# Optimization experiments

Measured on AMD Instinct MI355X. Metric: run time of the kernel, lower is better.

Reference implementation:

```python
import jax, jax.numpy as jnp
import numpy as np

B, S, DIM = 4, 2048, 1024
H, DH = 16, 64
INNER = H * DH  # 1024
SCALE = DH ** -0.5
NEG = -10000.0


def setup_inputs() -> dict:
    key = jax.random.key(0)
    k1, k2, k3, k4 = jax.random.split(key, 4)
    x = jax.random.normal(k1, (B, S, DIM), dtype=jnp.float32)
    w_qkv = jax.random.normal(k2, (DIM, 3 * INNER), dtype=jnp.float32) * (DIM ** -0.5)
    w_out = jax.random.normal(k3, (INNER, DIM), dtype=jnp.float32) * (INNER ** -0.5)
    b_out = jax.random.normal(k4, (DIM,), dtype=jnp.float32) * 0.01
    return {"x": x, "w_qkv": w_qkv, "w_out": w_out, "b_out": b_out}


def reference(x, w_qkv, w_out, b_out):
    b, s, _ = x.shape
    qkv = x @ w_qkv                                  # [b, s, 3*inner]
    q, k, v = jnp.split(qkv, 3, axis=-1)
    def heads(t):
        return t.reshape(b, s, H, DH).transpose(0, 2, 1, 3)  # [b, h, s, dh]
    q, k, v = heads(q), heads(k), heads(v)
    sim = jnp.einsum('bhid,bhjd->bhij', q, k)        # [b, h, s, s]
    i = jnp.arange(s)
    mask = jnp.where(i[None, :] <= i[:, None], 0.0, NEG).astype(sim.dtype)
    # NOTE: original scales (sim + mask), so mask bias is -10000*scale
    attn = jax.nn.softmax((sim + mask) * SCALE, axis=-1)
    out = jnp.einsum('bhij,bhjd->bhid', attn, v)     # [b, h, s, dh]
    out = out.transpose(0, 2, 1, 3).reshape(b, s, INNER)
    return out @ w_out + b_out
```

## Files before the change

kernel.cpp:

```cpp
#include <hip/hip_runtime.h>
#include <stdint.h>

typedef unsigned short u16;
typedef uint32_t u32;
typedef __attribute__((ext_vector_type(4))) float f32x4;
typedef __attribute__((ext_vector_type(16))) float f32x16;
typedef __attribute__((ext_vector_type(8))) short bf16x8;
typedef __attribute__((ext_vector_type(4))) u32 u32x4;

#define MFMA16(a,b,c) __builtin_amdgcn_mfma_f32_16x16x32_bf16((a),(b),(c),0,0,0)
#define MFMA32(a,b,c) __builtin_amdgcn_mfma_f32_32x32x16_bf16((a),(b),(c),0,0,0)
#define QSCALE 0.18033688011112042f
#define MASKB  -1803.3688011112042f
#define MBASE  -16.0f

__device__ __forceinline__ u16 f2bf(float f){
  union { float f; uint32_t u; } v; v.f = f;
  uint32_t r = v.u + 0x7fffu + ((v.u >> 16) & 1u);
  return (u16)(r >> 16);
}

__device__ __forceinline__ u32 cvtpk(float lo, float hi){
  u32 r;
  asm volatile("v_cvt_pk_bf16_f32 %0, %1, %2" : "=v"(r) : "v"(lo), "v"(hi));
  return r;
}

__device__ __forceinline__ void plswap(u32 &a, u32 &b){
  auto r = __builtin_amdgcn_permlane32_swap(a, b, false, false);
  union { decltype(r) v; u32 w[2]; } u; u.v = r;
  a = u.w[0]; b = u.w[1];
}

union U4 { u32x4 u; bf16x8 b; };
__device__ __forceinline__ bf16x8 mkfrag(u32 a, u32 b, u32 c, u32 d){
  U4 x; x.u = (u32x4){a,b,c,d}; return x.b;
}

__device__ __forceinline__ void gload16(const void* g, void* l){
  __builtin_amdgcn_global_load_lds(
      (const __attribute__((address_space(1))) void*)g,
      (__attribute__((address_space(3))) void*)l, 16, 0, 0);
}

__global__ __launch_bounds__(256) void prep_k(const float* __restrict__ x, u16* __restrict__ xb,
                                              const float* __restrict__ w_qkv, u16* __restrict__ wqkvT,
                                              const float* __restrict__ w_out, u16* __restrict__ woutT){
  __shared__ float tile[64][65];
  const int id = blockIdx.x, t = threadIdx.x;
  if (id < 8192){
    int i = id*256 + t;
    float4 v = reinterpret_cast<const float4*>(x)[i];
    ushort4 o;
    o.x = f2bf(v.x); o.y = f2bf(v.y); o.z = f2bf(v.z); o.w = f2bf(v.w);
    reinterpret_cast<ushort4*>(xb)[i] = o;
    return;
  }
  const float* in; u16* out; int R, C, bx, by;
  if (id < 8960){ int id2 = id - 8192; in = w_qkv; out = wqkvT; R = 1024; C = 3072; bx = id2 % 48; by = id2 / 48; }
  else          { int id3 = id - 8960; in = w_out; out = woutT; R = 1024; C = 1024; bx = id3 % 16; by = id3 / 16; }
  int c0 = bx*64, r0 = by*64;
  int cc = t & 63, rr = t >> 6;
  #pragma unroll
  for (int i=0;i<16;++i){ int r = rr + i*4; tile[r][cc] = in[(size_t)(r0+r)*C + c0+cc]; }
  __syncthreads();
  #pragma unroll
  for (int i=0;i<16;++i){ int r = rr + i*4; out[(size_t)(c0+r)*R + r0+cc] = f2bf(tile[cc][r]); }
}

__device__ __forceinline__ void gemm_core(const u16* __restrict__ A, const u16* __restrict__ Bt,
                                          int bm, int bn, char* lds, f32x4 (&acc)[4][4]){
  const int K = 1024;
  int tid = threadIdx.x, w = tid >> 6, l = tid & 63;
  int lrow = l & 15, lg = l >> 4;
  int wm = w >> 1, wn = w & 1;
  const u16* aSrc = A + (size_t)(bm*128 + w*32 + (l>>3))*K + (((l&7)^(l>>3))<<3);
  const u16* bSrc = Bt + (size_t)(bn*128 + w*32 + (l>>3))*K + (((l&7)^(l>>3))<<3);
  char* aDst = lds + w*4096;
  char* bDst = lds + 16384 + w*4096;
  for (int kk = 0; kk < 16; ++kk){
    __syncthreads();
    #pragma unroll
    for (int i=0;i<4;++i) gload16(aSrc + (size_t)i*8*K + kk*64, aDst + i*1024);
    #pragma unroll
    for (int i=0;i<4;++i) gload16(bSrc + (size_t)i*8*K + kk*64, bDst + i*1024);
    __syncthreads();
    #pragma unroll
    for (int ks=0; ks<2; ++ks){
      bf16x8 af[4], bfv[4];
      #pragma unroll
      for (int m=0;m<4;++m){
        int row = wm*64 + m*16 + lrow;
        af[m] = *reinterpret_cast<const bf16x8*>(lds + row*128 + (((ks*4+lg)^(row&7))<<4));
      }
      #pragma unroll
      for (int n=0;n<4;++n){
        int row = wn*64 + n*16 + lrow;
        bfv[n] = *reinterpret_cast<const bf16x8*>(lds + 16384 + row*128 + (((ks*4+lg)^(row&7))<<4));
      }
      #pragma unroll
      for (int m=0;m<4;++m){
        #pragma unroll
        for (int n=0;n<4;++n)
          acc[m][n] = MFMA16(af[m], bfv[n], acc[m][n]);
      }
    }
  }
}

__global__ __launch_bounds__(256,5) void gemm_qkv_k(const u16* __restrict__ A, const u16* __restrict__ Bt,
                                                    u16* __restrict__ qw, u16* __restrict__ kw,
                                                    u16* __restrict__ vtw){
  __shared__ __align__(16) char lds[32768];
  f32x4 acc[4][4];
  #pragma unroll
  for (int m=0;m<4;++m){
    #pragma unroll
    for (int n=0;n<4;++n) acc[m][n] = (f32x4){0.f,0.f,0.f,0.f};
  }
  int id = blockIdx.x + 24*blockIdx.y;
  int xcd = id & 7, s = id >> 3;
  int cb = s / 48, r = s % 48;
  int bm = xcd*8 + r/6;
  int bn = cb*6 + r%6;
  gemm_core(A, Bt, bm, bn, lds, acc);
  int tid = threadIdx.x, w = tid >> 6, l = tid & 63;
  int lrow = l & 15, lg = l >> 4;
  int wm = w >> 1, wn = w & 1;
  const int which = bn >> 3;
  if (which < 2){
    #pragma unroll
    for (int n=0;n<4;++n){
      int gcol = bn*128 + wn*64 + n*16 + lrow;
      int inner = gcol & 1023;
      int h = inner >> 6, d = inner & 63;
      #pragma unroll
      for (int m=0;m<4;++m){
        #pragma unroll
        for (int r2=0;r2<4;++r2){
          int grow = bm*128 + wm*64 + m*16 + lg*4 + r2;
          int b = grow >> 11, sq = grow & 2047;
          float v = acc[m][n][r2];
          if (which == 0)
            qw[((size_t)((b*16 + h)*2048 + sq))*64 + d] = f2bf(v * QSCALE);
          else
            kw[((size_t)((b*16 + h)*2048 + sq))*64 + d] = f2bf(v);
        }
      }
    }
  } else {
    __syncthreads();
    #pragma unroll
    for (int n=0;n<4;++n){
      int colL = wn*64 + n*16 + lrow;
      int swz = (colL & 7) << 4;
      #pragma unroll
      for (int m=0;m<4;++m){
        int rowL0 = wm*64 + m*16 + lg*4;
        ushort4 p;
        p.x = f2bf(acc[m][n][0]); p.y = f2bf(acc[m][n][1]);
        p.z = f2bf(acc[m][n][2]); p.w = f2bf(acc[m][n][3]);
        *reinterpret_cast<ushort4*>(lds + colL*256 + ((rowL0*2) ^ swz)) = p;
      }
    }
    __syncthreads();
    const int h0 = bn*2 - 32;
    const int grow0 = bm*128;
    const int b = grow0 >> 11, sq0 = grow0 & 2047;
    const int dp = tid >> 1;
    const int half = (tid & 1) * 128;
    const int h = h0 + (dp >> 6), d = dp & 63;
    const int swz = (dp & 7) << 4;
    u16* dst = vtw + ((size_t)((b*16 + h)*64 + d))*2048 + sq0 + half/2;
    #pragma unroll
    for (int i=0;i<8;++i){
      u32x4 v = *reinterpret_cast<const u32x4*>(lds + dp*256 + ((half + i*16) ^ swz));
      *reinterpret_cast<u32x4*>(dst + i*8) = v;
    }
  }
}

__global__ __launch_bounds__(256) void attn_k(const u16* __restrict__ Qw, const u16* __restrict__ Kw,
                                              const u16* __restrict__ VTw, u16* __restrict__ Ow){
  __shared__ __align__(16) char lds[32768];
  const int bh = blockIdx.x;
  const int y = blockIdx.y, yk = y >> 2, ya = y & 3;
  const int qb = (yk == 0) ? (15 - ya) : (yk == 1) ? (8 + ya) : (yk == 2) ? (4 + ya) : (3 - ya);
  const int tid = threadIdx.x, w = tid >> 6, l = tid & 63;
  const int lo = l & 31, hi = l >> 5;
  const size_t base = (size_t)bh * (2048*64);
  const int qw0 = qb*128 + w*32;
  const int q_l = qw0 + lo;

  bf16x8 qa[4];
  {
    const u16* qsrc = Qw + base + (size_t)q_l*64 + hi*8;
    #pragma unroll
    for (int ks=0; ks<4; ++ks) qa[ks] = *reinterpret_cast<const bf16x8*>(qsrc + ks*16);
  }

  const u32 ONE2 = 0x3F803F80u;
  const bf16x8 onesf = mkfrag(ONE2, ONE2, ONE2, ONE2);

  const int srow = tid >> 3;
  const int scs  = (tid & 7) ^ (srow & 7);
  const u16* kS = Kw  + base + (size_t)srow*64   + scs*8;
  const u16* vS = VTw + base + (size_t)srow*2048 + scs*8;

  f32x16 acc0 = {0,0,0,0,0,0,0,0,0,0,0,0,0,0,0,0};
  f32x16 acc1 = {0,0,0,0,0,0,0,0,0,0,0,0,0,0,0,0};
  f32x16 ls   = {0,0,0,0,0,0,0,0,0,0,0,0,0,0,0,0};
  const f32x16 minit = {MBASE,MBASE,MBASE,MBASE,MBASE,MBASE,MBASE,MBASE,
                        MBASE,MBASE,MBASE,MBASE,MBASE,MBASE,MBASE,MBASE};

  const int nt = qb*2 + 2;

  #define STAGE(buf, t) do { \
    int kv0_ = (t)*64; \
    gload16(kS + (size_t)kv0_*64,        lds + (buf)*16384 +     0 + w*1024); \
    gload16(kS + (size_t)(kv0_+32)*64,   lds + (buf)*16384 +  4096 + w*1024); \
    gload16(vS + kv0_,                   lds + (buf)*16384 +  8192 + w*1024); \
    gload16(vS + kv0_ + (size_t)32*2048, lds + (buf)*16384 + 12288 + w*1024); \
  } while(0)

  STAGE(0, 0);
  __syncthreads();

  int cur = 0;
  for (int t = 0; t < nt; ++t){
    if (t+1 < nt){
      if (cur) STAGE(0, t+1); else STAGE(1, t+1);
    }
    const int kv0 = t*64;
    const char* KB = lds + cur*16384;
    const char* VB = KB + 8192;
    if (kv0 + 63 <= qw0){
      f32x16 s0 = minit;
      f32x16 s1 = minit;
      __builtin_amdgcn_s_setprio(1);
      #pragma unroll
      for (int ks=0; ks<4; ++ks){
        int kr0 = lo, kr1 = 32 + lo;
        bf16x8 kf0 = *reinterpret_cast<const bf16x8*>(KB + kr0*128 + ((ks*32 + hi*16) ^ ((kr0&7)<<4)));
        bf16x8 kf1 = *reinterpret_cast<const bf16x8*>(KB + kr1*128 + ((ks*32 + hi*16) ^ ((kr1&7)<<4)));
        s0 = MFMA32(kf0, qa[ks], s0);
        s1 = MFMA32(kf1, qa[ks], s1);
      }
      __builtin_amdgcn_s_setprio(0);
      #pragma unroll
      for (int r=0; r<16; ++r) s0[r] = exp2f(s0[r]);
      #pragma unroll
      for (int r=0; r<16; ++r) s1[r] = exp2f(s1[r]);
      u32 wd0 = cvtpk(s0[0],s0[1]),   wd1 = cvtpk(s0[2],s0[3]);
      u32 wd2 = cvtpk(s0[4],s0[5]),   wd3 = cvtpk(s0[6],s0[7]);
      u32 wd4 = cvtpk(s0[8],s0[9]),   wd5 = cvtpk(s0[10],s0[11]);
      u32 wd6 = cvtpk(s0[12],s0[13]), wd7 = cvtpk(s0[14],s0[15]);
      u32 we0 = cvtpk(s1[0],s1[1]),   we1 = cvtpk(s1[2],s1[3]);
      u32 we2 = cvtpk(s1[4],s1[5]),   we3 = cvtpk(s1[6],s1[7]);
      u32 we4 = cvtpk(s1[8],s1[9]),   we5 = cvtpk(s1[10],s1[11]);
      u32 we6 = cvtpk(s1[12],s1[13]), we7 = cvtpk(s1[14],s1[15]);
      plswap(wd0, wd2); plswap(wd1, wd3); plswap(wd4, wd6); plswap(wd5, wd7);
      plswap(we0, we2); plswap(we1, we3); plswap(we4, we6); plswap(we5, we7);
      bf16x8 pf0 = mkfrag(wd0, wd1, wd2, wd3);
      bf16x8 pf1 = mkfrag(wd4, wd5, wd6, wd7);
      bf16x8 pf2 = mkfrag(we0, we1, we2, we3);
      bf16x8 pf3 = mkfrag(we4, we5, we6, we7);
      __builtin_amdgcn_s_setprio(1);
      {
        int vrow = lo;
        bf16x8 v0 = *reinterpret_cast<const bf16x8*>(VB + vrow*128 + ((      hi*16) ^ ((vrow&7)<<4)));
        bf16x8 v1 = *reinterpret_cast<const bf16x8*>(VB + vrow*128 + (( 32 + hi*16) ^ ((vrow&7)<<4)));
        bf16x8 v2 = *reinterpret_cast<const bf16x8*>(VB + vrow*128 + (( 64 + hi*16) ^ ((vrow&7)<<4)));
        bf16x8 v3 = *reinterpret_cast<const bf16x8*>(VB + vrow*128 + (( 96 + hi*16) ^ ((vrow&7)<<4)));
        acc0 = MFMA32(v0, pf0, acc0);
        acc0 = MFMA32(v1, pf1, acc0);
        acc0 = MFMA32(v2, pf2, acc0);
        acc0 = MFMA32(v3, pf3, acc0);
      }
      {
        int vrow = 32 + lo;
        bf16x8 v0 = *reinterpret_cast<const bf16x8*>(VB + vrow*128 + ((      hi*16) ^ ((vrow&7)<<4)));
        bf16x8 v1 = *reinterpret_cast<const bf16x8*>(VB + vrow*128 + (( 32 + hi*16) ^ ((vrow&7)<<4)));
        bf16x8 v2 = *reinterpret_cast<const bf16x8*>(VB + vrow*128 + (( 64 + hi*16) ^ ((vrow&7)<<4)));
        bf16x8 v3 = *reinterpret_cast<const bf16x8*>(VB + vrow*128 + (( 96 + hi*16) ^ ((vrow&7)<<4)));
        acc1 = MFMA32(v0, pf0, acc1);
        acc1 = MFMA32(v1, pf1, acc1);
        acc1 = MFMA32(v2, pf2, acc1);
        acc1 = MFMA32(v3, pf3, acc1);
      }
      ls = MFMA32(onesf, pf0, ls);
      ls = MFMA32(onesf, pf1, ls);
      ls = MFMA32(onesf, pf2, ls);
      ls = MFMA32(onesf, pf3, ls);
      __builtin_amdgcn_s_setprio(0);
    } else if (kv0 < qw0 + 32){
      #pragma unroll
      for (int t2=0; t2<2; ++t2){
        const int kvs0 = kv0 + t2*32;
        if (kvs0 < qw0 + 32){
          f32x16 s = minit;
          __builtin_amdgcn_s_setprio(1);
          #pragma unroll
          for (int ks=0; ks<4; ++ks){
            int krow = t2*32 + lo;
            bf16x8 kf = *reinterpret_cast<const bf16x8*>(KB + krow*128 + ((ks*32 + hi*16) ^ ((krow&7)<<4)));
            s = MFMA32(kf, qa[ks], s);
          }
          __builtin_amdgcn_s_setprio(0);
          if (kvs0 + 31 > qw0){
            #pragma unroll
            for (int r=0; r<16; ++r){
              int kvg = kvs0 + (r&3) + 8*(r>>2) + 4*hi;
              if (kvg > q_l) s[r] += MASKB;
            }
          }
          #pragma unroll
          for (int r=0; r<16; ++r) s[r] = exp2f(s[r]);
          u32 wd0 = cvtpk(s[0], s[1]),   wd1 = cvtpk(s[2], s[3]);
          u32 wd2 = cvtpk(s[4], s[5]),   wd3 = cvtpk(s[6], s[7]);
          u32 wd4 = cvtpk(s[8], s[9]),   wd5 = cvtpk(s[10], s[11]);
          u32 wd6 = cvtpk(s[12], s[13]), wd7 = cvtpk(s[14], s[15]);
          plswap(wd0, wd2); plswap(wd1, wd3);
          plswap(wd4, wd6); plswap(wd5, wd7);
          bf16x8 pf0 = mkfrag(wd0, wd1, wd2, wd3);
          bf16x8 pf1 = mkfrag(wd4, wd5, wd6, wd7);
          __builtin_amdgcn_s_setprio(1);
          {
            int vrow = lo;
            bf16x8 v0 = *reinterpret_cast<const bf16x8*>(VB + vrow*128 + ((t2*64 +      hi*16) ^ ((vrow&7)<<4)));
            bf16x8 v1 = *reinterpret_cast<const bf16x8*>(VB + vrow*128 + ((t2*64 + 32 + hi*16) ^ ((vrow&7)<<4)));
            acc0 = MFMA32(v0, pf0, acc0);
            acc0 = MFMA32(v1, pf1, acc0);
          }
          {
            int vrow = 32 + lo;
            bf16x8 v0 = *reinterpret_cast<const bf16x8*>(VB + vrow*128 + ((t2*64 +      hi*16) ^ ((vrow&7)<<4)));
            bf16x8 v1 = *reinterpret_cast<const bf16x8*>(VB + vrow*128 + ((t2*64 + 32 + hi*16) ^ ((vrow&7)<<4)));
            acc1 = MFMA32(v0, pf0, acc1);
            acc1 = MFMA32(v1, pf1, acc1);
          }
          ls = MFMA32(onesf, pf0, ls);
          ls = MFMA32(onesf, pf1, ls);
          __builtin_amdgcn_s_setprio(0);
        }
      }
    }
    __syncthreads();
    cur ^= 1;
  }
  #undef STAGE

  char* T = lds + w*4096;
  float inv = 1.0f / ls[0];
  #pragma unroll
  for (int i=0; i<8; ++i){
    int d = (2*i & 3) + 8*(2*i >> 2) + 4*hi;
    u32 wv0 = cvtpk(acc0[2*i]*inv, acc0[2*i+1]*inv);
    *reinterpret_cast<u32*>(T + lo*128 + ((d*2) ^ ((lo&7)<<4))) = wv0;
    u32 wv1 = cvtpk(acc1[2*i]*inv, acc1[2*i+1]*inv);
    *reinterpret_cast<u32*>(T + lo*128 + (((d+32)*2) ^ ((lo&7)<<4))) = wv1;
  }
  __syncthreads();
  const int b = bh >> 4, h = bh & 15;
  #pragma unroll
  for (int i=0; i<4; ++i){
    int q = i*8 + (l>>3), slot = l&7;
    bf16x8 v = *reinterpret_cast<const bf16x8*>(T + q*128 + ((slot*16) ^ ((q&7)<<4)));
    int sq = qb*128 + w*32 + q;
    *reinterpret_cast<bf16x8*>(Ow + ((size_t)(b*2048 + sq))*1024 + h*64 + slot*8) = v;
  }
}

__global__ __launch_bounds__(256,4) void gemm_out_k(const u16* __restrict__ A, const u16* __restrict__ Bt,
                                                    const float* __restrict__ bias_p, float* __restrict__ out){
  __shared__ __align__(16) char lds[32768];
  f32x4 acc[4][4];
  #pragma unroll
  for (int m=0;m<4;++m){
    #pragma unroll
    for (int n=0;n<4;++n) acc[m][n] = (f32x4){0.f,0.f,0.f,0.f};
  }
  int id = blockIdx.x + 8*blockIdx.y;
  int nid = (id & 7)*64 + (id >> 3);
  int bn = nid % 8, bm = nid / 8;
  gemm_core(A, Bt, bm, bn, lds, acc);
  int tid = threadIdx.x, w = tid >> 6, l = tid & 63;
  int lrow = l & 15, lg = l >> 4;
  int wm = w >> 1, wn = w & 1;
  #pragma unroll
  for (int n=0;n<4;++n){
    int gcol = bn*128 + wn*64 + n*16 + lrow;
    float bias = bias_p[gcol];
    #pragma unroll
    for (int m=0;m<4;++m){
      #pragma unroll
      for (int r=0;r<4;++r){
        int grow = bm*128 + wm*64 + m*16 + lg*4 + r;
        __builtin_nontemporal_store(acc[m][n][r] + bias, out + (size_t)grow*1024 + gcol);
      }
    }
  }
}

extern "C" void kernel_launch(void* const* d_in, const int* in_sizes, int n_in,
                              void* d_out, int out_size, void* d_ws, size_t ws_size,
                              hipStream_t stream){
  (void)in_sizes; (void)n_in; (void)out_size; (void)ws_size;
  const float* x     = (const float*)d_in[0];
  const float* w_qkv = (const float*)d_in[1];
  const float* w_out = (const float*)d_in[2];
  const float* b_out = (const float*)d_in[3];
  float* out = (float*)d_out;
  char* ws = (char*)d_ws;
  u16* xb    = (u16*)(ws + 0);
  u16* wqkvT = (u16*)(ws + 16777216);
  u16* woutT = (u16*)(ws + 23068672);
  u16* qw    = (u16*)(ws + 25165824);
  u16* kw    = (u16*)(ws + 41943040);
  u16* vtw   = (u16*)(ws + 58720256);
  u16* attn  = (u16*)(ws + 75497472);

  prep_k<<<9216, 256, 0, stream>>>(x, xb, w_qkv, wqkvT, w_out, woutT);
  gemm_qkv_k<<<dim3(24,64), 256, 0, stream>>>(xb, wqkvT, qw, kw, vtw);
  attn_k<<<dim3(64,16), 256, 0, stream>>>(qw, kw, vtw, attn);
  gemm_out_k<<<dim3(8,64), 256, 0, stream>>>(attn, woutT, b_out, out);
}
```

Before: 168.8 us.

## Split long causal attention rows across KV chunks and merge partials

The causal attention grid goes from 16 to 30 work items per head. Query blocks 6 and above have their KV range split into 2 or 3 chunks using lookup tables, with the aim of balancing per-block work and raising occupancy. Each chunk writes an unnormalized bf16 partial output plus its row sums, and a new merge kernel adds the partials and normalizes. This relies on a fixed max-free softmax base (MBASE) so partials can be summed directly. The cost is an extra launch, extra global traffic, and bf16 rounding of unnormalized partials. Partials reuse the xb workspace region, which is dead by then.

```diff
diff --git a/kernel.cpp b/kernel.cpp
--- a/kernel.cpp
+++ b/kernel.cpp
@@ -14,10 +14,19 @@
 #define MASKB  -1803.3688011112042f
 #define MBASE  -16.0f
 
+__constant__ int QB_T[30] = {5,11,11,10,10,15,15,4,9,9,13,14,14,14,15,8,8,12,12,13,13,3,7,7,12,6,6,2,1,0};
+__constant__ int T0_T[30] = {0,0,12,0,11,0,11,0,0,10,0,0,10,20,22,0,9,0,9,10,19,0,0,8,18,0,7,0,0,0};
+__constant__ int T1_T[30] = {12,12,24,11,22,11,22,10,10,20,10,10,20,30,32,9,18,9,18,19,28,8,8,16,26,7,14,6,4,2};
+__constant__ int C_T[30]  = {0,0,1,0,1,0,1,0,0,1,0,0,1,2,2,0,1,0,1,1,2,0,0,1,2,0,1,0,0,0};
+
 __device__ __forceinline__ u16 f2bf(float f){
   union { float f; uint32_t u; } v; v.f = f;
   uint32_t r = v.u + 0x7fffu + ((v.u >> 16) & 1u);
   return (u16)(r >> 16);
+}
+
+__device__ __forceinline__ float bf2f(u16 x){
+  union { u32 u; float f; } v; v.u = ((u32)x) << 16; return v.f;
 }
 
 __device__ __forceinline__ u32 cvtpk(float lo, float hi){
@@ -181,11 +190,12 @@
 }
 
 __global__ __launch_bounds__(256) void attn_k(const u16* __restrict__ Qw, const u16* __restrict__ Kw,
-                                              const u16* __restrict__ VTw, u16* __restrict__ Ow){
+                                              const u16* __restrict__ VTw, u16* __restrict__ Ow,
+                                              u16* __restrict__ slots, float* __restrict__ l_arr){
   __shared__ __align__(16) char lds[32768];
   const int bh = blockIdx.x;
-  const int y = blockIdx.y, yk = y >> 2, ya = y & 3;
-  const int qb = (yk == 0) ? (15 - ya) : (yk == 1) ? (8 + ya) : (yk == 2) ? (4 + ya) : (3 - ya);
+  const int yc = blockIdx.y;
+  const int qb = QB_T[yc], t0c = T0_T[yc], t1c = T1_T[yc], ck = C_T[yc];
   const int tid = threadIdx.x, w = tid >> 6, l = tid & 63;
   const int lo = l & 31, hi = l >> 5;
   const size_t base = (size_t)bh * (2048*64);
@@ -212,8 +222,6 @@
   f32x16 ls   = {0,0,0,0,0,0,0,0,0,0,0,0,0,0,0,0};
   const f32x16 minit = {MBASE,MBASE,MBASE,MBASE,MBASE,MBASE,MBASE,MBASE,
                         MBASE,MBASE,MBASE,MBASE,MBASE,MBASE,MBASE,MBASE};
-
-  const int nt = qb*2 + 2;
 
   #define STAGE(buf, t) do { \
     int kv0_ = (t)*64; \
@@ -223,12 +231,12 @@
     gload16(vS + kv0_ + (size_t)32*2048, lds + (buf)*16384 + 12288 + w*1024); \
   } while(0)
 
-  STAGE(0, 0);
+  STAGE(0, t0c);
   __syncthreads();
 
   int cur = 0;
-  for (int t = 0; t < nt; ++t){
-    if (t+1 < nt){
+  for (int t = t0c; t < t1c; ++t){
+    if (t+1 < t1c){
       if (cur) STAGE(0, t+1); else STAGE(1, t+1);
     }
     const int kv0 = t*64;
@@ -350,8 +358,28 @@
   }
   #undef STAGE
 
+  const int b = bh >> 4, h = bh & 15;
+  float inv;
+  u16* dstbase;
+  int pitch;
+  if (qb < 6){
+    inv = 1.0f / ls[0];
+    dstbase = Ow + ((size_t)(b*2048 + qb*128))*1024 + h*64;
+    pitch = 1024;
+  } else {
+    int li = (qb <= 11) ? ((qb-6)*2 + ck) : (12 + (qb-12)*3 + ck);
+    if (hi == 0) l_arr[((size_t)bh*24 + li)*128 + w*32 + lo] = ls[0];
+    inv = 1.0f;
+    if (ck == 0){
+      dstbase = Ow + ((size_t)(b*2048 + qb*128))*1024 + h*64;
+      pitch = 1024;
+    } else {
+      int e = (qb <= 11) ? (qb-6) : (6 + (qb-12)*2 + (ck-1));
+      dstbase = slots + ((size_t)bh*14 + e)*8192;
+      pitch = 64;
+    }
+  }
   char* T = lds + w*4096;
-  float inv = 1.0f / ls[0];
   #pragma unroll
   for (int i=0; i<8; ++i){
     int d = (2*i & 3) + 8*(2*i >> 2) + 4*hi;
@@ -361,13 +389,57 @@
     *reinterpret_cast<u32*>(T + lo*128 + (((d+32)*2) ^ ((lo&7)<<4))) = wv1;
   }
   __syncthreads();
-  const int b = bh >> 4, h = bh & 15;
   #pragma unroll
   for (int i=0; i<4; ++i){
     int q = i*8 + (l>>3), slot = l&7;
     bf16x8 v = *reinterpret_cast<const bf16x8*>(T + q*128 + ((slot*16) ^ ((q&7)<<4)));
-    int sq = qb*128 + w*32 + q;
-    *reinterpret_cast<bf16x8*>(Ow + ((size_t)(b*2048 + sq))*1024 + h*64 + slot*8) = v;
+    int row = w*32 + q;
+    *reinterpret_cast<bf16x8*>(dstbase + (size_t)row*pitch + slot*8) = v;
+  }
+}
+
+__global__ __launch_bounds__(256) void merge_k(u16* __restrict__ attn, const u16* __restrict__ slots,
+                                               const float* __restrict__ l_arr){
+  const int bid = blockIdx.x;
+  const int bh = bid & 63, qi = bid >> 6;
+  const int qb = 6 + qi;
+  const int tid = threadIdx.x;
+  const int r = tid >> 1, hf = (tid & 1)*32;
+  const int b = bh >> 4, h = bh & 15;
+  u16* ap = attn + ((size_t)(b*2048 + qb*128 + r))*1024 + h*64 + hf;
+  const float* lb = l_arr + (size_t)bh*24*128;
+  const size_t sbase = (size_t)bh*14*8192;
+  float lt;
+  const u16 *e0, *e1 = nullptr;
+  if (qb <= 11){
+    lt = lb[((qb-6)*2+0)*128 + r] + lb[((qb-6)*2+1)*128 + r];
+    e0 = slots + sbase + (size_t)(qb-6)*8192 + r*64 + hf;
+  } else {
+    int li0 = 12 + (qb-12)*3;
+    lt = lb[(size_t)li0*128 + r] + lb[(size_t)(li0+1)*128 + r] + lb[(size_t)(li0+2)*128 + r];
+    int eb = 6 + (qb-12)*2;
+    e0 = slots + sbase + (size_t)eb*8192 + r*64 + hf;
+    e1 = slots + sbase + (size_t)(eb+1)*8192 + r*64 + hf;
+  }
+  float inv = 1.0f / lt;
+  #pragma unroll
+  for (int i=0;i<4;++i){
+    bf16x8 a  = *reinterpret_cast<const bf16x8*>(ap + i*8);
+    bf16x8 p0 = *reinterpret_cast<const bf16x8*>(e0 + i*8);
+    bf16x8 p1;
+    if (e1) p1 = *reinterpret_cast<const bf16x8*>(e1 + i*8);
+    ushort4 o0, o1;
+    u16 ov[8];
+    #pragma unroll
+    for (int j=0;j<8;++j){
+      float v = bf2f((u16)a[j]) + bf2f((u16)p0[j]);
+      if (e1) v += bf2f((u16)p1[j]);
+      ov[j] = f2bf(v * inv);
+    }
+    o0.x = ov[0]; o0.y = ov[1]; o0.z = ov[2]; o0.w = ov[3];
+    o1.x = ov[4]; o1.y = ov[5]; o1.z = ov[6]; o1.w = ov[7];
+    *reinterpret_cast<ushort4*>(ap + i*8)     = o0;
+    *reinterpret_cast<ushort4*>(ap + i*8 + 4) = o1;
   }
 }
 
@@ -412,7 +484,9 @@
   const float* b_out = (const float*)d_in[3];
   float* out = (float*)d_out;
   char* ws = (char*)d_ws;
-  u16* xb    = (u16*)(ws + 0);
+  u16*   xb     = (u16*)(ws + 0);
+  u16*   slots  = (u16*)(ws + 0);
+  float* l_arr  = (float*)(ws + 14680064);
   u16* wqkvT = (u16*)(ws + 16777216);
   u16* woutT = (u16*)(ws + 23068672);
   u16* qw    = (u16*)(ws + 25165824);
@@ -422,6 +496,7 @@
 
   prep_k<<<9216, 256, 0, stream>>>(x, xb, w_qkv, wqkvT, w_out, woutT);
   gemm_qkv_k<<<dim3(24,64), 256, 0, stream>>>(xb, wqkvT, qw, kw, vtw);
-  attn_k<<<dim3(64,16), 256, 0, stream>>>(qw, kw, vtw, attn);
+  attn_k<<<dim3(64,30), 256, 0, stream>>>(qw, kw, vtw, attn, slots, l_arr);
+  merge_k<<<640, 256, 0, stream>>>(attn, slots, l_arr);
   gemm_out_k<<<dim3(8,64), 256, 0, stream>>>(attn, woutT, b_out, out);
 }
```

Result: slower. 176.5 us (+4.6%).
